# Performance work log

Hardware: AMD Instinct MI355X
Metric: run time of the kernel (lower is better)

Reference implementation:

```python
import jax, jax.numpy as jnp
import numpy as np

N_NODES = 20000
N_EDGES = 320000
F_IN = 512
F_OUT = 1024
N_GRAPHS = 64


def gcn_conv(x, src, dst, ew, W, b, n_nodes):
    xw = x @ W  # [N, Fout]
    loop = jnp.arange(n_nodes)
    s = jnp.concatenate([src, loop])
    d = jnp.concatenate([dst, loop])
    w = jnp.concatenate([ew, jnp.ones((n_nodes,), dtype=x.dtype)])
    deg = jax.ops.segment_sum(w, d, num_segments=n_nodes)  # in-degree by weight
    dinv = jnp.where(deg > 0, jax.lax.rsqrt(deg), 0.0).astype(x.dtype)
    norm = dinv[s] * w * dinv[d]  # [E+N]
    msg = norm[:, None] * xw[s]  # [E+N, Fout]
    out = jax.ops.segment_sum(msg, d, num_segments=n_nodes)
    return out + b


def mean_pool(x, batch, n_graphs):
    sums = jax.ops.segment_sum(x, batch, num_segments=n_graphs)
    cnt = jax.ops.segment_sum(jnp.ones((x.shape[0],), dtype=x.dtype), batch, num_segments=n_graphs)
    return sums / jnp.maximum(cnt, 1.0)[:, None]


def setup_inputs() -> dict:
    key = jax.random.key(0)
    ks = jax.random.split(key, 8)
    node_features = jax.random.normal(ks[0], (N_NODES, F_IN), dtype=jnp.float32)
    edge_index = jax.random.randint(ks[1], (2, N_EDGES), 0, N_NODES, dtype=jnp.int64)
    edge_weight = jax.random.uniform(ks[2], (N_EDGES,), dtype=jnp.float32)
    batch = jnp.sort(jax.random.randint(ks[3], (N_NODES,), 0, N_GRAPHS, dtype=jnp.int64))
    # Glorot-style params for the two GCNConv layers
    W1 = jax.random.normal(ks[4], (F_IN, F_OUT), dtype=jnp.float32) / np.sqrt(F_IN)
    b1 = jnp.zeros((F_OUT,), dtype=jnp.float32)
    W2 = jax.random.normal(ks[5], (F_OUT, F_OUT), dtype=jnp.float32) / np.sqrt(F_OUT)
    b2 = jnp.zeros((F_OUT,), dtype=jnp.float32)
    return {"node_features": node_features, "edge_index": edge_index,
            "edge_weight": edge_weight, "batch": batch,
            "W1": W1, "b1": b1, "W2": W2, "b2": b2}


def reference(node_features, edge_index, edge_weight, batch, W1, b1, W2, b2):
    n_nodes = node_features.shape[0]
    src, dst = edge_index[0], edge_index[1]
    h = jax.nn.relu(gcn_conv(node_features, src, dst, edge_weight, W1, b1, n_nodes))
    h = jax.nn.relu(gcn_conv(h, src, dst, edge_weight, W2, b2, n_nodes))
    return mean_pool(h, batch, N_GRAPHS)  # [G, F_OUT]
```

## Files before the change

kernel.cpp:

```cpp
#include <hip/hip_runtime.h>

#define N_NODES 20000
#define N_PAD   20480
#define N_EDGES 320000
#define F_IN 512
#define F_OUT 1024
#define N_GRAPHS 64
#define ESTRIDE 64

typedef __attribute__((ext_vector_type(8))) short bf16x8;
typedef __attribute__((ext_vector_type(4))) float f32x4;
typedef __attribute__((ext_vector_type(8))) unsigned short ushort8v;

static __device__ __forceinline__ unsigned short f2bf(float f) {
    unsigned int u = __float_as_uint(f);
    u = (u + 0x7fff + ((u >> 16) & 1)) >> 16;
    return (unsigned short)u;
}
static __device__ __forceinline__ float bf2f(unsigned short s) {
    return __uint_as_float(((unsigned int)s) << 16);
}

__global__ void k_setup(float* deg, int* cursor, float* out,
                        const int* __restrict__ batch, int* gstart,
                        unsigned int* __restrict__ csre) {
    int i = blockIdx.x * 256 + threadIdx.x;
    if (i < N_NODES) { deg[i] = 1.0f; cursor[i] = 0; }
    if (i < N_GRAPHS * F_OUT) out[i] = 0.f;
    if (i <= N_GRAPHS) {
        if (i == N_GRAPHS) gstart[i] = N_NODES;
        else {
            int lo = 0, hi = N_NODES;
            while (lo < hi) {
                int mid = (lo + hi) >> 1;
                if (batch[mid] < i) lo = mid + 1; else hi = mid;
            }
            gstart[i] = lo;
        }
    }
    for (int t = i; t < N_NODES * ESTRIDE; t += 65536) csre[t] = 0u;
}

#define NB_E    ((N_EDGES + 255) / 256)
#define NB_WT   ((F_OUT / 32) * (F_IN / 32 + F_OUT / 32))
#define NB_CX   (N_PAD * (F_IN / 8) / 256)
__global__ __launch_bounds__(256) void k_pre(const int* __restrict__ dst,
                                             const float* __restrict__ ew,
                                             float* deg,
                                             const float* __restrict__ W1,
                                             unsigned short* __restrict__ Wt1,
                                             const float* __restrict__ W2,
                                             unsigned short* __restrict__ Wt2,
                                             const float* __restrict__ x,
                                             unsigned short* __restrict__ xb) {
    __shared__ float tile[32][33];
    const int bid = blockIdx.x;
    if (bid < NB_E) {
        int e = bid * 256 + threadIdx.x;
        if (e < N_EDGES) atomicAdd(&deg[dst[e]], ew[e]);
    } else if (bid < NB_E + NB_WT) {
        int cid = bid - NB_E;
        int by = cid >> 5;
        int n0 = (cid & 31) * 32;
        const float* W; unsigned short* Wt; int K, k0;
        if (by < F_IN / 32) { W = W1; Wt = Wt1; K = F_IN;  k0 = by * 32; }
        else                { W = W2; Wt = Wt2; K = F_OUT; k0 = (by - F_IN / 32) * 32; }
        int tx = threadIdx.x & 31;
        int ty = threadIdx.x >> 5;
#pragma unroll
        for (int i = 0; i < 32; i += 8)
            tile[ty + i][tx] = W[(size_t)(k0 + ty + i) * F_OUT + n0 + tx];
        __syncthreads();
#pragma unroll
        for (int i = 0; i < 32; i += 8)
            Wt[(size_t)(n0 + ty + i) * K + k0 + tx] = f2bf(tile[tx][ty + i]);
    } else {
        int idx = (bid - NB_E - NB_WT) * 256 + threadIdx.x;
        int row = idx >> 6;
        int c8 = (idx & 63) * 8;
        if (row >= N_PAD) return;
        ushort8v v;
        if (row < N_NODES) {
            const float* p = &x[(size_t)row * F_IN + c8];
#pragma unroll
            for (int i = 0; i < 8; i++) v[i] = f2bf(p[i]);
        } else {
#pragma unroll
            for (int i = 0; i < 8; i++) v[i] = 0;
        }
        *(ushort8v*)&xb[(size_t)row * F_IN + c8] = v;
    }
}

__global__ void k_fill(const int* __restrict__ src, const int* __restrict__ dst,
                       const float* __restrict__ ew, const float* __restrict__ deg,
                       int* cursor, unsigned int* __restrict__ csre) {
    int e = blockIdx.x * 256 + threadIdx.x;
    if (e < N_EDGES) {
        int d = dst[e], s = src[e];
        int pos = atomicAdd(&cursor[d], 1);
        if (pos < ESTRIDE) {
            float w = rsqrtf(deg[s]) * ew[e] * rsqrtf(deg[d]);
            csre[d * ESTRIDE + pos] = ((unsigned int)f2bf(w) << 16) | (unsigned int)s;
        }
    }
}

__global__ __launch_bounds__(256) void k_aggr_slab(const unsigned short* __restrict__ xin,
                                                   const float* __restrict__ deg,
                                                   const int* __restrict__ cursor,
                                                   const unsigned int* __restrict__ csre,
                                                   const float* __restrict__ bias,
                                                   unsigned short* __restrict__ outp,
                                                   int F, int act) {
    const int bid = blockIdx.x;
    const int slab = bid & 7;
    const int ng = (bid >> 3) * 4 + (threadIdx.x >> 6);
    const int lane = threadIdx.x & 63;
    const int n = ng * 8 + (lane >> 3);
    const int c = blockIdx.y * 512 + slab * 64 + (lane & 7) * 8;

    if (n >= N_NODES) {
        ushort8v z;
#pragma unroll
        for (int i = 0; i < 8; i++) z[i] = 0;
        *(ushort8v*)&outp[(size_t)n * F + c] = z;
        return;
    }

    const char* xb_ = (const char*)xin;
    const unsigned shB = (F == 512) ? 10u : 11u;
    const unsigned c2 = (unsigned)(c * 2);

    const float di = rsqrtf(deg[n]);
    const float wself = di * di;
    float a[8];
    {
        ushort8v v = *(const ushort8v*)(xb_ + (((unsigned)n << shB) + c2));
#pragma unroll
        for (int i = 0; i < 8; i++) a[i] = bf2f(v[i]) * wself;
    }

    const unsigned int* ce = csre + (size_t)n * ESTRIDE;
    const int cnt = min(cursor[n], ESTRIDE);
    const int cnt4 = (cnt + 3) & ~3;

    if (cnt4 > 0) {
        uint4 m0 = *(const uint4*)&ce[0];
        uint4 m1 = (4 < cnt4) ? *(const uint4*)&ce[4] : m0;
        ushort8v u0 = *(const ushort8v*)(xb_ + (((m0.x & 0xFFFFu) << shB) + c2));
        ushort8v u1 = *(const ushort8v*)(xb_ + (((m0.y & 0xFFFFu) << shB) + c2));
        ushort8v u2 = *(const ushort8v*)(xb_ + (((m0.z & 0xFFFFu) << shB) + c2));
        ushort8v u3 = *(const ushort8v*)(xb_ + (((m0.w & 0xFFFFu) << shB) + c2));

        for (int j = 4; j < cnt4; j += 4) {
            ushort8v v0 = *(const ushort8v*)(xb_ + (((m1.x & 0xFFFFu) << shB) + c2));
            ushort8v v1 = *(const ushort8v*)(xb_ + (((m1.y & 0xFFFFu) << shB) + c2));
            ushort8v v2 = *(const ushort8v*)(xb_ + (((m1.z & 0xFFFFu) << shB) + c2));
            ushort8v v3 = *(const ushort8v*)(xb_ + (((m1.w & 0xFFFFu) << shB) + c2));
            const int jn = (j + 4 < cnt4) ? j + 4 : 0;
            uint4 m2 = *(const uint4*)&ce[jn];
            {
                float w0 = __uint_as_float(m0.x & 0xFFFF0000u);
                float w1 = __uint_as_float(m0.y & 0xFFFF0000u);
                float w2 = __uint_as_float(m0.z & 0xFFFF0000u);
                float w3 = __uint_as_float(m0.w & 0xFFFF0000u);
#pragma unroll
                for (int i = 0; i < 8; i++) {
                    a[i] += w0 * bf2f(u0[i]);
                    a[i] += w1 * bf2f(u1[i]);
                    a[i] += w2 * bf2f(u2[i]);
                    a[i] += w3 * bf2f(u3[i]);
                }
            }
            m0 = m1; m1 = m2;
            u0 = v0; u1 = v1; u2 = v2; u3 = v3;
        }
        {
            float w0 = __uint_as_float(m0.x & 0xFFFF0000u);
            float w1 = __uint_as_float(m0.y & 0xFFFF0000u);
            float w2 = __uint_as_float(m0.z & 0xFFFF0000u);
            float w3 = __uint_as_float(m0.w & 0xFFFF0000u);
#pragma unroll
            for (int i = 0; i < 8; i++) {
                a[i] += w0 * bf2f(u0[i]);
                a[i] += w1 * bf2f(u1[i]);
                a[i] += w2 * bf2f(u2[i]);
                a[i] += w3 * bf2f(u3[i]);
            }
        }
    }

    ushort8v r;
    if (act) {
#pragma unroll
        for (int i = 0; i < 8; i++) r[i] = f2bf(fmaxf(a[i] + bias[c + i], 0.f));
    } else {
#pragma unroll
        for (int i = 0; i < 8; i++) r[i] = f2bf(a[i]);
    }
    *(ushort8v*)&outp[(size_t)n * F + c] = r;
}

__global__ __launch_bounds__(256, 3) void k_gemm_sb(const unsigned short* __restrict__ A,
                                                    const unsigned short* __restrict__ Bt,
                                                    unsigned short* __restrict__ C, int K,
                                                    const float* __restrict__ bias, int act) {
    __shared__ short As[128 * 64];
    __shared__ short Bs[128 * 64];
    const int bid = blockIdx.x;
    const int xcd = bid & 7;
    const int i2 = bid >> 3;
    const int colb = i2 & 7;
    const int rowb = xcd * 20 + (i2 >> 3);
    const int row0 = rowb * 128;
    const int col0 = colb * 128;

    const int tid = threadIdx.x;
    const int lane = tid & 63;
    const int wave = tid >> 6;
    const int wm = wave >> 1, wn = wave & 1;
    const int l16 = lane & 15;
    const int kq = lane >> 4;

    const int NT = K >> 6;
    f32x4 acc[4][4] = {};

    for (int t = 0; t < NT; ++t) {
        const int k0 = t * 64;
#pragma unroll
        for (int it = 0; it < 4; it++) {
            int q = it * 256 + tid;
            int r = q >> 3;
            int g = (q & 7) ^ (r & 7);
            __builtin_amdgcn_global_load_lds(
                (const __attribute__((address_space(1))) void*)&A[(size_t)(row0 + r) * K + k0 + g * 8],
                (__attribute__((address_space(3))) void*)&As[q * 8], 16, 0, 0);
            __builtin_amdgcn_global_load_lds(
                (const __attribute__((address_space(1))) void*)&Bt[(size_t)(col0 + r) * K + k0 + g * 8],
                (__attribute__((address_space(3))) void*)&Bs[q * 8], 16, 0, 0);
        }
        __syncthreads();

#pragma unroll
        for (int ks = 0; ks < 2; ks++) {
            bf16x8 af[4], bfr[4];
#pragma unroll
            for (int fr = 0; fr < 4; fr++) {
                int r = wm * 64 + fr * 16 + l16;
                int g = (ks * 4 + kq) ^ (r & 7);
                af[fr] = *(const bf16x8*)&As[(r * 8 + g) * 8];
            }
#pragma unroll
            for (int fc = 0; fc < 4; fc++) {
                int r = wn * 64 + fc * 16 + l16;
                int g = (ks * 4 + kq) ^ (r & 7);
                bfr[fc] = *(const bf16x8*)&Bs[(r * 8 + g) * 8];
            }
            __builtin_amdgcn_s_setprio(1);
#pragma unroll
            for (int fr = 0; fr < 4; fr++)
#pragma unroll
                for (int fc = 0; fc < 4; fc++)
                    acc[fr][fc] = __builtin_amdgcn_mfma_f32_16x16x32_bf16(
                        af[fr], bfr[fc], acc[fr][fc], 0, 0, 0);
            __builtin_amdgcn_s_setprio(0);
        }
        __syncthreads();
    }

#pragma unroll
    for (int fr = 0; fr < 4; fr++) {
        int m0 = row0 + wm * 64 + fr * 16 + kq * 4;
#pragma unroll
        for (int fc = 0; fc < 4; fc++) {
            int n = col0 + wn * 64 + fc * 16 + l16;
            float bv = act ? bias[n] : 0.f;
#pragma unroll
            for (int reg = 0; reg < 4; reg++) {
                float v = acc[fr][fc][reg];
                if (act) v = fmaxf(v + bv, 0.f);
                C[(size_t)(m0 + reg) * F_OUT + n] = f2bf(v);
            }
        }
    }
}

__global__ __launch_bounds__(64) void k_pool_g(const unsigned short* __restrict__ h,
                                               const int* __restrict__ gstart,
                                               float* __restrict__ out) {
    const int g = blockIdx.x >> 4;
    const int slab = blockIdx.x & 15;
    const int lane = threadIdx.x;
    const int c = slab * 64 + (lane & 7) * 8;
    const int r0 = gstart[g], r1 = gstart[g + 1];

    float a[8] = {};
    for (int r = r0 + (lane >> 3); r < r1; r += 8) {
        ushort8v v = *(const ushort8v*)&h[(size_t)r * F_OUT + c];
#pragma unroll
        for (int i = 0; i < 8; i++) a[i] += bf2f(v[i]);
    }
#pragma unroll
    for (int m = 8; m < 64; m <<= 1)
#pragma unroll
        for (int i = 0; i < 8; i++) a[i] += __shfl_xor(a[i], m, 64);

    if ((lane >> 3) == 0) {
        const float inv = 1.0f / (float)max(r1 - r0, 1);
#pragma unroll
        for (int i = 0; i < 8; i++)
            out[(size_t)g * F_OUT + c + i] = a[i] * inv;
    }
}

extern "C" void kernel_launch(void* const* d_in, const int* in_sizes, int n_in,
                              void* d_out, int out_size, void* d_ws, size_t ws_size,
                              hipStream_t stream) {
    const float* x    = (const float*)d_in[0];
    const int* ei     = (const int*)d_in[1];
    const float* ew   = (const float*)d_in[2];
    const int* batch  = (const int*)d_in[3];
    const float* W1   = (const float*)d_in[4];
    const float* b1   = (const float*)d_in[5];
    const float* W2   = (const float*)d_in[6];
    const float* b2   = (const float*)d_in[7];
    float* out = (float*)d_out;

    const int* src = ei;
    const int* dst = ei + N_EDGES;

    char* ws = (char*)d_ws;
    const size_t SZ_XB  = (size_t)N_PAD * F_IN * 2;
    const size_t SZ_AX  = (size_t)N_PAD * F_IN * 2;
    const size_t SZ_WT1 = (size_t)F_OUT * F_IN * 2;
    const size_t SZ_WT2 = (size_t)F_OUT * F_OUT * 2;
    const size_t SZ_B   = (size_t)N_PAD * F_OUT * 2;
    unsigned short* xb  = (unsigned short*)(ws);
    unsigned short* ax  = (unsigned short*)(ws + SZ_XB);
    unsigned short* Wt1 = (unsigned short*)(ws + SZ_XB + SZ_AX);
    unsigned short* Wt2 = (unsigned short*)(ws + SZ_XB + SZ_AX + SZ_WT1);
    unsigned short* h1  = (unsigned short*)(ws + SZ_XB + SZ_AX + SZ_WT1 + SZ_WT2);
    unsigned short* xw2 = (unsigned short*)(ws + SZ_XB + SZ_AX + SZ_WT1 + SZ_WT2 + SZ_B);
    unsigned short* h2  = (unsigned short*)(ws);
    size_t off = SZ_XB + SZ_AX + SZ_WT1 + SZ_WT2 + 2 * SZ_B;
    auto alloc = [&](size_t bytes) -> void* {
        void* p = ws + off;
        off += (bytes + 255) & ~(size_t)255;
        return p;
    };
    float*        deg    = (float*)       alloc((size_t)N_NODES * 4);
    int*          cursor = (int*)         alloc((size_t)N_NODES * 4);
    unsigned int* csre   = (unsigned int*)alloc((size_t)N_NODES * ESTRIDE * 4);
    int*          gstart = (int*)         alloc((size_t)(N_GRAPHS + 1) * 4);

    k_setup<<<(N_GRAPHS * F_OUT + 255) / 256, 256, 0, stream>>>(deg, cursor, out, batch, gstart, csre);
    k_pre<<<NB_E + NB_WT + NB_CX, 256, 0, stream>>>(dst, ew, deg, W1, Wt1, W2, Wt2, x, xb);
    k_fill<<<NB_E, 256, 0, stream>>>(src, dst, ew, deg, cursor, csre);
    k_aggr_slab<<<dim3((N_PAD / 32) * 8, 1), 256, 0, stream>>>(xb, deg, cursor, csre,
                                                               (const float*)nullptr, ax, F_IN, 0);
    const int gemm_blocks = (N_PAD / 128) * (F_OUT / 128);
    k_gemm_sb<<<gemm_blocks, 256, 0, stream>>>(ax, Wt1, h1, F_IN, b1, 1);
    k_gemm_sb<<<gemm_blocks, 256, 0, stream>>>(h1, Wt2, xw2, F_OUT, (const float*)nullptr, 0);
    k_aggr_slab<<<dim3((N_PAD / 32) * 8, 2), 256, 0, stream>>>(xw2, deg, cursor, csre, b2, h2, F_OUT, 1);
    k_pool_g<<<N_GRAPHS * 16, 64, 0, stream>>>(h2, gstart, out);
}
```

Before: 312.4 us.

## Triple-buffer GEMM LDS tiles with K=32 stages and vmcnt-based prefetch

```diff
diff --git a/kernel.cpp b/kernel.cpp
--- a/kernel.cpp
+++ b/kernel.cpp
@@ -202,12 +202,12 @@
     *(ushort8v*)&outp[(size_t)n * F + c] = r;
 }
 
-__global__ __launch_bounds__(256, 3) void k_gemm_sb(const unsigned short* __restrict__ A,
+__global__ __launch_bounds__(256, 3) void k_gemm_r3(const unsigned short* __restrict__ A,
                                                     const unsigned short* __restrict__ Bt,
                                                     unsigned short* __restrict__ C, int K,
                                                     const float* __restrict__ bias, int act) {
-    __shared__ short As[128 * 64];
-    __shared__ short Bs[128 * 64];
+    __shared__ short As[3][128 * 32];
+    __shared__ short Bs[3][128 * 32];
     const int bid = blockIdx.x;
     const int xcd = bid & 7;
     const int i2 = bid >> 3;
@@ -223,50 +223,75 @@
     const int l16 = lane & 15;
     const int kq = lane >> 4;
 
-    const int NT = K >> 6;
+    const int NT = K >> 5;
     f32x4 acc[4][4] = {};
 
-    for (int t = 0; t < NT; ++t) {
-        const int k0 = t * 64;
-#pragma unroll
-        for (int it = 0; it < 4; it++) {
+    auto stage = [&](int t, int sl) {
+        const int k0 = t * 32;
+#pragma unroll
+        for (int it = 0; it < 2; it++) {
             int q = it * 256 + tid;
-            int r = q >> 3;
-            int g = (q & 7) ^ (r & 7);
+            int rr = q >> 3;
+            int G = (q & 7) ^ (rr & 7);
+            int r = rr * 2 + (G >> 2);
+            int g = G & 3;
             __builtin_amdgcn_global_load_lds(
                 (const __attribute__((address_space(1))) void*)&A[(size_t)(row0 + r) * K + k0 + g * 8],
-                (__attribute__((address_space(3))) void*)&As[q * 8], 16, 0, 0);
+                (__attribute__((address_space(3))) void*)&As[sl][q * 8], 16, 0, 0);
             __builtin_amdgcn_global_load_lds(
                 (const __attribute__((address_space(1))) void*)&Bt[(size_t)(col0 + r) * K + k0 + g * 8],
-                (__attribute__((address_space(3))) void*)&Bs[q * 8], 16, 0, 0);
-        }
-        __syncthreads();
-
-#pragma unroll
-        for (int ks = 0; ks < 2; ks++) {
-            bf16x8 af[4], bfr[4];
-#pragma unroll
-            for (int fr = 0; fr < 4; fr++) {
-                int r = wm * 64 + fr * 16 + l16;
-                int g = (ks * 4 + kq) ^ (r & 7);
-                af[fr] = *(const bf16x8*)&As[(r * 8 + g) * 8];
-            }
-#pragma unroll
-            for (int fc = 0; fc < 4; fc++) {
-                int r = wn * 64 + fc * 16 + l16;
-                int g = (ks * 4 + kq) ^ (r & 7);
-                bfr[fc] = *(const bf16x8*)&Bs[(r * 8 + g) * 8];
-            }
-            __builtin_amdgcn_s_setprio(1);
-#pragma unroll
-            for (int fr = 0; fr < 4; fr++)
-#pragma unroll
-                for (int fc = 0; fc < 4; fc++)
-                    acc[fr][fc] = __builtin_amdgcn_mfma_f32_16x16x32_bf16(
-                        af[fr], bfr[fc], acc[fr][fc], 0, 0, 0);
-            __builtin_amdgcn_s_setprio(0);
-        }
-        __syncthreads();
+                (__attribute__((address_space(3))) void*)&Bs[sl][q * 8], 16, 0, 0);
+        }
+    };
+
+    stage(0, 0);
+    if (NT > 1) {
+        stage(1, 1);
+        asm volatile("s_waitcnt vmcnt(4)" ::: "memory");
+    } else {
+        asm volatile("s_waitcnt vmcnt(0)" ::: "memory");
+    }
+    __builtin_amdgcn_s_barrier();
+    __builtin_amdgcn_sched_barrier(0);
+
+    int s = 0;
+    for (int t = 0; t < NT; ++t) {
+        int s2 = s + 2; if (s2 >= 3) s2 -= 3;
+        if (t + 2 < NT) stage(t + 2, s2);
+
+        const short* Asl = As[s];
+        const short* Bsl = Bs[s];
+        bf16x8 af[4], bfr[4];
+#pragma unroll
+        for (int fr = 0; fr < 4; fr++) {
+            int r = wm * 64 + fr * 16 + l16;
+            int rr = r >> 1;
+            int G = (r & 1) * 4 + kq;
+            af[fr] = *(const bf16x8*)&Asl[(rr * 8 + (G ^ (rr & 7))) * 8];
+        }
+#pragma unroll
+        for (int fc = 0; fc < 4; fc++) {
+            int r = wn * 64 + fc * 16 + l16;
+            int rr = r >> 1;
+            int G = (r & 1) * 4 + kq;
+            bfr[fc] = *(const bf16x8*)&Bsl[(rr * 8 + (G ^ (rr & 7))) * 8];
+        }
+        __builtin_amdgcn_s_setprio(1);
+#pragma unroll
+        for (int fr = 0; fr < 4; fr++)
+#pragma unroll
+            for (int fc = 0; fc < 4; fc++)
+                acc[fr][fc] = __builtin_amdgcn_mfma_f32_16x16x32_bf16(
+                    af[fr], bfr[fc], acc[fr][fc], 0, 0, 0);
+        __builtin_amdgcn_s_setprio(0);
+
+        if (t < NT - 1) {
+            if (t + 2 < NT) asm volatile("s_waitcnt vmcnt(4)" ::: "memory");
+            else            asm volatile("s_waitcnt vmcnt(0)" ::: "memory");
+            __builtin_amdgcn_s_barrier();
+            __builtin_amdgcn_sched_barrier(0);
+        }
+        s = s + 1; if (s >= 3) s -= 3;
     }
 
 #pragma unroll
@@ -360,8 +385,8 @@
     k_aggr_slab<<<dim3((N_PAD / 32) * 8, 1), 256, 0, stream>>>(xb, deg, cursor, csre,
                                                                (const float*)nullptr, ax, F_IN, 0);
     const int gemm_blocks = (N_PAD / 128) * (F_OUT / 128);
-    k_gemm_sb<<<gemm_blocks, 256, 0, stream>>>(ax, Wt1, h1, F_IN, b1, 1);
-    k_gemm_sb<<<gemm_blocks, 256, 0, stream>>>(h1, Wt2, xw2, F_OUT, (const float*)nullptr, 0);
+    k_gemm_r3<<<gemm_blocks, 256, 0, stream>>>(ax, Wt1, h1, F_IN, b1, 1);
+    k_gemm_r3<<<gemm_blocks, 256, 0, stream>>>(h1, Wt2, xw2, F_OUT, (const float*)nullptr, 0);
     k_aggr_slab<<<dim3((N_PAD / 32) * 8, 2), 256, 0, stream>>>(xw2, deg, cursor, csre, b2, h2, F_OUT, 1);
     k_pool_g<<<N_GRAPHS * 16, 64, 0, stream>>>(h2, gstart, out);
 }
```

Measured after the change: 328.5 us. 1.05x slower.
